# Kernel optimization log

Measured on AMD Instinct MI355X. Metric: run time of the kernel, lower is better.

## Reference

```python
import jax, jax.numpy as jnp
import numpy as np

N_EMBD = 1024
HEAD_SIZE = 64
WINDOW = 64
N_GLOBAL = 64
N_RANDOM = 64
B, T = 8, 2048


def setup_inputs() -> dict:
    key = jax.random.key(0)
    kx, kc, kk, kq, kv = jax.random.split(key, 5)
    x = jax.random.normal(kx, (B, T, N_EMBD), dtype=jnp.float32)
    random_cols = jax.random.randint(kc, (T, N_RANDOM), 0, T)
    s = 1.0 / np.sqrt(N_EMBD)
    Wk = jax.random.normal(kk, (HEAD_SIZE, N_EMBD), dtype=jnp.float32) * s
    Wq = jax.random.normal(kq, (HEAD_SIZE, N_EMBD), dtype=jnp.float32) * s
    Wv = jax.random.normal(kv, (HEAD_SIZE, N_EMBD), dtype=jnp.float32) * s
    return {"x": x, "random_cols": random_cols, "Wk": Wk, "Wq": Wq, "Wv": Wv}


def _bigbird_mask(Tlen, random_cols):
    rows = jnp.arange(Tlen)[:, None]
    cols = jnp.arange(Tlen)[None, :]
    causal = rows >= cols
    local = (cols >= rows - WINDOW + 1) & (cols <= rows)
    glob = (rows < N_GLOBAL) | (cols < N_GLOBAL)
    rand = jnp.zeros((Tlen, Tlen), dtype=bool).at[
        jnp.arange(Tlen)[:, None], random_cols].set(True)
    return (local | glob | rand) & causal  # [T, T] bool


def reference(x, random_cols, Wk, Wq, Wv):
    # projections (Linear, no bias): [B,T,C] @ [C,H] -> [B,T,H]
    k = jnp.einsum('btc,hc->bth', x, Wk)
    q = jnp.einsum('btc,hc->bth', x, Wq)
    v = jnp.einsum('btc,hc->bth', x, Wv)
    scale = 1.0 / jnp.sqrt(jnp.asarray(HEAD_SIZE, x.dtype))
    scores = jnp.einsum('bqh,bkh->bqk', q, k) * scale  # [B,T,T]
    mask = _bigbird_mask(x.shape[1], random_cols)
    scores = jnp.where(mask[None, :, :], scores, -jnp.inf)
    weights = jax.nn.softmax(scores, axis=-1)
    out = jnp.einsum('bqk,bkh->bqh', weights, v)  # [B,T,H]
    return out
```

## Files before the change

kernel.cpp:

```cpp
#include <hip/hip_runtime.h>
#include <math.h>

#define T_DIM 2048
#define C_DIM 1024
#define H_DIM 64
#define M_TOTAL 16384
#define NQKV 192

typedef __bf16 bf16x8 __attribute__((ext_vector_type(8)));
typedef float f32x4 __attribute__((ext_vector_type(4)));
typedef unsigned short u16x8 __attribute__((ext_vector_type(8)));

__device__ __forceinline__ unsigned short f2bf(float f) {
    unsigned u = __float_as_uint(f);
    unsigned r = (u + 0x7FFFu + ((u >> 16) & 1u)) >> 16;
    return (unsigned short)r;
}
__device__ __forceinline__ float bf2f(unsigned short u) {
    return __uint_as_float(((unsigned)u) << 16);
}
__device__ __forceinline__ unsigned pack_bf2(float f0, float f1) {
    unsigned u0 = __float_as_uint(f0) + 0x8000u;
    unsigned u1 = __float_as_uint(f1) + 0x8000u;
    return __builtin_amdgcn_perm(u1, u0, 0x07060302u);
}
__device__ __forceinline__ uint4 cvt8(float4 a, float4 b) {
    return make_uint4(pack_bf2(a.x, a.y), pack_bf2(a.z, a.w),
                      pack_bf2(b.x, b.y), pack_bf2(b.z, b.w));
}

__global__ __launch_bounds__(512) void proj_kernel(
    const float* __restrict__ x,
    const float* __restrict__ Wk,
    const float* __restrict__ Wq,
    const float* __restrict__ Wv,
    unsigned short* __restrict__ qkv)
{
    __shared__ unsigned short Ab[64 * 64];
    __shared__ unsigned short Bb[192 * 64];

    const int m0 = blockIdx.x * 64;
    const int t  = threadIdx.x;
    const int wv = t >> 6, ln = t & 63;
    const int mfr = ln & 15, kq = ln >> 4;
    const int r0 = (wv & 1) * 32;
    const int c0 = (wv >> 1) * 48;

    const int srow  = t >> 3;
    const int sk8   = (t & 7) * 8;
    const int skoff = sk8 ^ ((srow & 7) * 8);

    const float* gp[4] = {
        x  + (size_t)(m0 + srow) * C_DIM + sk8,
        Wk + (size_t)srow * C_DIM + sk8,
        Wq + (size_t)srow * C_DIM + sk8,
        Wv + (size_t)srow * C_DIM + sk8 };
    unsigned short* lp[4] = {
        &Ab[srow * 64 + skoff],
        &Bb[srow * 64 + skoff],
        &Bb[(srow + 64) * 64 + skoff],
        &Bb[(srow + 128) * 64 + skoff] };

    f32x4 acc[2][3] = {};

    float4 ra[4], rb[4];
    #pragma unroll
    for (int s = 0; s < 4; ++s) {
        ra[s] = *(const float4*)(gp[s]);
        rb[s] = *(const float4*)(gp[s] + 4);
    }

    for (int kc = 0; kc < C_DIM; kc += 64) {
        __syncthreads();
        #pragma unroll
        for (int s = 0; s < 4; ++s)
            *(uint4*)lp[s] = cvt8(ra[s], rb[s]);
        if (kc + 64 < C_DIM) {
            #pragma unroll
            for (int s = 0; s < 4; ++s) {
                ra[s] = *(const float4*)(gp[s] + kc + 64);
                rb[s] = *(const float4*)(gp[s] + kc + 68);
            }
        }
        __syncthreads();
        #pragma unroll
        for (int ks = 0; ks < 64; ks += 32) {
            bf16x8 af[2], bf[3];
            #pragma unroll
            for (int a = 0; a < 2; ++a) {
                int row = r0 + a * 16 + mfr;
                af[a] = *(const bf16x8*)&Ab[row * 64 + ((ks + kq * 8) ^ ((row & 7) * 8))];
            }
            #pragma unroll
            for (int b2 = 0; b2 < 3; ++b2) {
                int row = c0 + b2 * 16 + mfr;
                bf[b2] = *(const bf16x8*)&Bb[row * 64 + ((ks + kq * 8) ^ ((row & 7) * 8))];
            }
            #pragma unroll
            for (int a = 0; a < 2; ++a)
                #pragma unroll
                for (int b2 = 0; b2 < 3; ++b2)
                    acc[a][b2] = __builtin_amdgcn_mfma_f32_16x16x32_bf16(
                        af[a], bf[b2], acc[a][b2], 0, 0, 0);
        }
    }

    #pragma unroll
    for (int a = 0; a < 2; ++a)
        #pragma unroll
        for (int b2 = 0; b2 < 3; ++b2)
            #pragma unroll
            for (int r = 0; r < 4; ++r) {
                int row = m0 + r0 + a * 16 + kq * 4 + r;
                int col = c0 + b2 * 16 + mfr;
                qkv[(size_t)row * NQKV + col] = f2bf(acc[a][b2][r]);
            }
}

__global__ __launch_bounds__(256) void attn_kernel(
    const unsigned short* __restrict__ qkv,
    const int*  __restrict__ rnd,
    float* __restrict__ out)
{
    const int wv = threadIdx.x >> 6;
    const int ln = threadIdx.x & 63;
    const int b  = blockIdx.x & 7;
    const int i  = ((blockIdx.x >> 3) << 2) + wv;
    const int bi = b * T_DIM + i;

    __shared__ int2     cl_all[4][192];
    __shared__ unsigned bm_all[4][64];
    int2*     cl = cl_all[wv];
    unsigned* bm = bm_all[wv];

    bm[ln] = 0u;

    int  j0 = i - ln;            bool v0 = (j0 >= 0); if (!v0) j0 = 0;
    int  j1 = ln;                bool v1 = (j1 < i - 63);
    int  j2 = rnd[i * 64 + ln];  bool v2 = (j2 < i - 63) && (j2 >= 64);
    if (v2) {
        unsigned old = atomicOr(&bm[j2 >> 5], 1u << (j2 & 31));
        v2 = ((old >> (j2 & 31)) & 1u) == 0u;
    }
    cl[ln]       = make_int2(j0, 0);
    cl[64 + ln]  = make_int2(j1, 0);
    cl[128 + ln] = make_int2(j2, 0);

    const int e8 = (ln & 7) * 8;
    const int gg = ln >> 3;
    u16x8 qraw = *(const u16x8*)(qkv + (size_t)bi * NQKV + 64 + e8);
    float qr[8];
    #pragma unroll
    for (int e = 0; e < 8; ++e) qr[e] = bf2f(qraw[e]);

    const unsigned short* kb = qkv + (size_t)b * T_DIM * NQKV;

    #pragma unroll
    for (int n = 0; n < 24; n += 4) {
        int jj[4];
        #pragma unroll
        for (int u = 0; u < 4; ++u) jj[u] = cl[(n + u) * 8 + gg].x;
        u16x8 kv[4];
        #pragma unroll
        for (int u = 0; u < 4; ++u)
            kv[u] = *(const u16x8*)(kb + (size_t)jj[u] * NQKV + e8);
        #pragma unroll
        for (int u = 0; u < 4; ++u) {
            float p = 0.f;
            #pragma unroll
            for (int e = 0; e < 8; ++e) p = fmaf(qr[e], bf2f(kv[u][e]), p);
            p += __shfl_xor(p, 1);
            p += __shfl_xor(p, 2);
            p += __shfl_xor(p, 4);
            if ((ln & 7) == 0) cl[(n + u) * 8 + gg].y = __float_as_int(p);
        }
    }

    float s0 = __int_as_float(cl[ln].y);
    float s1 = __int_as_float(cl[64 + ln].y);
    float s2 = __int_as_float(cl[128 + ln].y);
    s0 = v0 ? s0 * 0.125f : -1e30f;
    s1 = v1 ? s1 * 0.125f : -1e30f;
    s2 = v2 ? s2 * 0.125f : -1e30f;

    float mx = fmaxf(s0, fmaxf(s1, s2));
    #pragma unroll
    for (int m = 32; m; m >>= 1) mx = fmaxf(mx, __shfl_xor(mx, m));
    float e0 = v0 ? __expf(s0 - mx) : 0.f;
    float e1 = v1 ? __expf(s1 - mx) : 0.f;
    float e2 = v2 ? __expf(s2 - mx) : 0.f;
    float sum = e0 + e1 + e2;
    #pragma unroll
    for (int m = 32; m; m >>= 1) sum += __shfl_xor(sum, m);

    cl[ln].y       = __float_as_int(e0);
    cl[64 + ln].y  = __float_as_int(e1);
    cl[128 + ln].y = __float_as_int(e2);

    const unsigned short* vb = kb + 128;
    float acc[8] = {};
    #pragma unroll
    for (int bt = 0; bt < 3; ++bt) {
        int2 p[8];
        #pragma unroll
        for (int c = 0; c < 8; ++c) p[c] = cl[(bt * 8 + c) * 8 + gg];
        u16x8 vvv[8];
        #pragma unroll
        for (int c = 0; c < 8; ++c)
            vvv[c] = *(const u16x8*)(vb + (size_t)p[c].x * NQKV + e8);
        #pragma unroll
        for (int c = 0; c < 8; ++c) {
            float w = __int_as_float(p[c].y);
            #pragma unroll
            for (int e = 0; e < 8; ++e)
                acc[e] = fmaf(w, bf2f(vvv[c][e]), acc[e]);
        }
    }
    #pragma unroll
    for (int m = 8; m <= 32; m <<= 1)
        #pragma unroll
        for (int e = 0; e < 8; ++e)
            acc[e] += __shfl_xor(acc[e], m);

    if (ln < 8) {
        float inv = 1.f / sum;
        float* op = &out[(size_t)bi * H_DIM + e8];
        *(float4*)op       = make_float4(acc[0]*inv, acc[1]*inv, acc[2]*inv, acc[3]*inv);
        *(float4*)(op + 4) = make_float4(acc[4]*inv, acc[5]*inv, acc[6]*inv, acc[7]*inv);
    }
}

extern "C" void kernel_launch(void* const* d_in, const int* in_sizes, int n_in,
                              void* d_out, int out_size, void* d_ws, size_t ws_size,
                              hipStream_t stream) {
    const float* x   = (const float*)d_in[0];
    const int*   rnd = (const int*)  d_in[1];
    const float* Wk  = (const float*)d_in[2];
    const float* Wq  = (const float*)d_in[3];
    const float* Wv  = (const float*)d_in[4];
    float* out = (float*)d_out;
    unsigned short* qkv = (unsigned short*)d_ws;

    proj_kernel<<<M_TOTAL / 64, 512, 0, stream>>>(x, Wk, Wq, Wv, qkv);
    attn_kernel<<<M_TOTAL / 4, 256, 0, stream>>>(qkv, rnd, out);
}
```

Before: 150.5 us.

## Stage global and local-window K/V rows in LDS shared by 16 queries per block

Each attention block now handles 16 consecutive queries (4 per wave) and first copies the 64 global-token K/V rows plus the union of their local-window rows into shared memory with a padded row stride. Local and global score and value gathers then read from LDS, and only the random columns still gather from global memory. This cuts repeated global and L2 traffic for the overlapping windows. In exchange it adds an up-front staging pass, a block-wide barrier, about 40 KB of LDS per block that may limit occupancy, and a quarter as many blocks.

```diff
diff --git a/kernel.cpp b/kernel.cpp
--- a/kernel.cpp
+++ b/kernel.cpp
@@ -6,6 +6,7 @@
 #define H_DIM 64
 #define M_TOTAL 16384
 #define NQKV 192
+#define LROW 140
 
 typedef __bf16 bf16x8 __attribute__((ext_vector_type(8)));
 typedef float f32x4 __attribute__((ext_vector_type(4)));
@@ -19,6 +20,8 @@
 __device__ __forceinline__ float bf2f(unsigned short u) {
     return __uint_as_float(((unsigned)u) << 16);
 }
+__device__ __forceinline__ float blo(unsigned u) { return __uint_as_float(u << 16); }
+__device__ __forceinline__ float bhi(unsigned u) { return __uint_as_float(u & 0xFFFF0000u); }
 __device__ __forceinline__ unsigned pack_bf2(float f0, float f1) {
     unsigned u0 = __float_as_uint(f0) + 0x8000u;
     unsigned u1 = __float_as_uint(f1) + 0x8000u;
@@ -122,111 +125,187 @@
     const int*  __restrict__ rnd,
     float* __restrict__ out)
 {
-    const int wv = threadIdx.x >> 6;
-    const int ln = threadIdx.x & 63;
-    const int b  = blockIdx.x & 7;
-    const int i  = ((blockIdx.x >> 3) << 2) + wv;
-    const int bi = b * T_DIM + i;
-
+    __shared__ unsigned short Ks[143 * LROW];
     __shared__ int2     cl_all[4][192];
     __shared__ unsigned bm_all[4][64];
+
+    const int t  = threadIdx.x;
+    const int wv = t >> 6;
+    const int ln = t & 63;
+    const int b  = blockIdx.x & 7;
+    const int i0 = (blockIdx.x >> 3) << 4;
+    const int Lb = (i0 - 63 > 64) ? (i0 - 63) : 64;
+    int nL = i0 + 16 - Lb; if (nL < 0) nL = 0;
+    const int S_rows = 64 + nL;
+
+    const unsigned short* kb = qkv + (size_t)b * T_DIM * NQKV;
+
+    {
+        const int u  = t >> 3;
+        const int c8 = (t & 7) * 8;
+        for (int s = u; s < S_rows; s += 32) {
+            int j = (s < 64) ? s : (Lb + (s - 64));
+            const unsigned short* src = kb + (size_t)j * NQKV;
+            uint4 kk = *(const uint4*)(src + c8);
+            uint4 vv = *(const uint4*)(src + 128 + c8);
+            *(uint2*)&Ks[s * LROW + c8]          = make_uint2(kk.x, kk.y);
+            *(uint2*)&Ks[s * LROW + c8 + 4]      = make_uint2(kk.z, kk.w);
+            *(uint2*)&Ks[s * LROW + 64 + c8]     = make_uint2(vv.x, vv.y);
+            *(uint2*)&Ks[s * LROW + 64 + c8 + 4] = make_uint2(vv.z, vv.w);
+        }
+    }
+    __syncthreads();
+
     int2*     cl = cl_all[wv];
     unsigned* bm = bm_all[wv];
-
-    bm[ln] = 0u;
-
-    int  j0 = i - ln;            bool v0 = (j0 >= 0); if (!v0) j0 = 0;
-    int  j1 = ln;                bool v1 = (j1 < i - 63);
-    int  j2 = rnd[i * 64 + ln];  bool v2 = (j2 < i - 63) && (j2 >= 64);
-    if (v2) {
-        unsigned old = atomicOr(&bm[j2 >> 5], 1u << (j2 & 31));
-        v2 = ((old >> (j2 & 31)) & 1u) == 0u;
-    }
-    cl[ln]       = make_int2(j0, 0);
-    cl[64 + ln]  = make_int2(j1, 0);
-    cl[128 + ln] = make_int2(j2, 0);
-
     const int e8 = (ln & 7) * 8;
     const int gg = ln >> 3;
-    u16x8 qraw = *(const u16x8*)(qkv + (size_t)bi * NQKV + 64 + e8);
-    float qr[8];
-    #pragma unroll
-    for (int e = 0; e < 8; ++e) qr[e] = bf2f(qraw[e]);
-
-    const unsigned short* kb = qkv + (size_t)b * T_DIM * NQKV;
-
-    #pragma unroll
-    for (int n = 0; n < 24; n += 4) {
-        int jj[4];
-        #pragma unroll
-        for (int u = 0; u < 4; ++u) jj[u] = cl[(n + u) * 8 + gg].x;
-        u16x8 kv[4];
-        #pragma unroll
-        for (int u = 0; u < 4; ++u)
-            kv[u] = *(const u16x8*)(kb + (size_t)jj[u] * NQKV + e8);
-        #pragma unroll
-        for (int u = 0; u < 4; ++u) {
-            float p = 0.f;
-            #pragma unroll
-            for (int e = 0; e < 8; ++e) p = fmaf(qr[e], bf2f(kv[u][e]), p);
-            p += __shfl_xor(p, 1);
-            p += __shfl_xor(p, 2);
-            p += __shfl_xor(p, 4);
-            if ((ln & 7) == 0) cl[(n + u) * 8 + gg].y = __float_as_int(p);
-        }
-    }
-
-    float s0 = __int_as_float(cl[ln].y);
-    float s1 = __int_as_float(cl[64 + ln].y);
-    float s2 = __int_as_float(cl[128 + ln].y);
-    s0 = v0 ? s0 * 0.125f : -1e30f;
-    s1 = v1 ? s1 * 0.125f : -1e30f;
-    s2 = v2 ? s2 * 0.125f : -1e30f;
-
-    float mx = fmaxf(s0, fmaxf(s1, s2));
-    #pragma unroll
-    for (int m = 32; m; m >>= 1) mx = fmaxf(mx, __shfl_xor(mx, m));
-    float e0 = v0 ? __expf(s0 - mx) : 0.f;
-    float e1 = v1 ? __expf(s1 - mx) : 0.f;
-    float e2 = v2 ? __expf(s2 - mx) : 0.f;
-    float sum = e0 + e1 + e2;
-    #pragma unroll
-    for (int m = 32; m; m >>= 1) sum += __shfl_xor(sum, m);
-
-    cl[ln].y       = __float_as_int(e0);
-    cl[64 + ln].y  = __float_as_int(e1);
-    cl[128 + ln].y = __float_as_int(e2);
-
-    const unsigned short* vb = kb + 128;
-    float acc[8] = {};
-    #pragma unroll
-    for (int bt = 0; bt < 3; ++bt) {
-        int2 p[8];
-        #pragma unroll
-        for (int c = 0; c < 8; ++c) p[c] = cl[(bt * 8 + c) * 8 + gg];
-        u16x8 vvv[8];
-        #pragma unroll
-        for (int c = 0; c < 8; ++c)
-            vvv[c] = *(const u16x8*)(vb + (size_t)p[c].x * NQKV + e8);
-        #pragma unroll
-        for (int c = 0; c < 8; ++c) {
-            float w = __int_as_float(p[c].y);
+
+    for (int qq = 0; qq < 4; ++qq) {
+        const int i  = i0 + wv * 4 + qq;
+        const int bi = b * T_DIM + i;
+
+        bm[ln] = 0u;
+
+        int  j0 = i - ln;            bool v0 = (j0 >= 0); if (!v0) j0 = 0;
+        int  j1 = ln;                bool v1 = (j1 < i - 63);
+        int  j2 = rnd[i * 64 + ln];  bool v2 = (j2 < i - 63) && (j2 >= 64);
+        if (v2) {
+            unsigned old = atomicOr(&bm[j2 >> 5], 1u << (j2 & 31));
+            v2 = ((old >> (j2 & 31)) & 1u) == 0u;
+        }
+        cl[ln]       = make_int2(j0, 0);
+        cl[64 + ln]  = make_int2(j1, 0);
+        cl[128 + ln] = make_int2(j2, 0);
+
+        uint4 qv4 = *(const uint4*)(qkv + (size_t)bi * NQKV + 64 + e8);
+        float qr[8] = { blo(qv4.x), bhi(qv4.x), blo(qv4.y), bhi(qv4.y),
+                        blo(qv4.z), bhi(qv4.z), blo(qv4.w), bhi(qv4.w) };
+
+        #pragma unroll
+        for (int n = 0; n < 16; n += 4) {
+            int sl[4];
+            #pragma unroll
+            for (int u = 0; u < 4; ++u) {
+                int j = cl[(n + u) * 8 + gg].x;
+                sl[u] = (j < 64) ? j : (64 + j - Lb);
+            }
+            uint2 ka[4], kc[4];
+            #pragma unroll
+            for (int u = 0; u < 4; ++u) {
+                ka[u] = *(const uint2*)&Ks[sl[u] * LROW + e8];
+                kc[u] = *(const uint2*)&Ks[sl[u] * LROW + e8 + 4];
+            }
+            #pragma unroll
+            for (int u = 0; u < 4; ++u) {
+                float p = 0.f;
+                p = fmaf(qr[0], blo(ka[u].x), p); p = fmaf(qr[1], bhi(ka[u].x), p);
+                p = fmaf(qr[2], blo(ka[u].y), p); p = fmaf(qr[3], bhi(ka[u].y), p);
+                p = fmaf(qr[4], blo(kc[u].x), p); p = fmaf(qr[5], bhi(kc[u].x), p);
+                p = fmaf(qr[6], blo(kc[u].y), p); p = fmaf(qr[7], bhi(kc[u].y), p);
+                p += __shfl_xor(p, 1);
+                p += __shfl_xor(p, 2);
+                p += __shfl_xor(p, 4);
+                if ((ln & 7) == 0) cl[(n + u) * 8 + gg].y = __float_as_int(p);
+            }
+        }
+        #pragma unroll
+        for (int n = 16; n < 24; n += 4) {
+            int jj[4];
+            #pragma unroll
+            for (int u = 0; u < 4; ++u) jj[u] = cl[(n + u) * 8 + gg].x;
+            u16x8 kv[4];
+            #pragma unroll
+            for (int u = 0; u < 4; ++u)
+                kv[u] = *(const u16x8*)(kb + (size_t)jj[u] * NQKV + e8);
+            #pragma unroll
+            for (int u = 0; u < 4; ++u) {
+                float p = 0.f;
+                #pragma unroll
+                for (int e = 0; e < 8; ++e) p = fmaf(qr[e], bf2f(kv[u][e]), p);
+                p += __shfl_xor(p, 1);
+                p += __shfl_xor(p, 2);
+                p += __shfl_xor(p, 4);
+                if ((ln & 7) == 0) cl[(n + u) * 8 + gg].y = __float_as_int(p);
+            }
+        }
+
+        float s0 = __int_as_float(cl[ln].y);
+        float s1 = __int_as_float(cl[64 + ln].y);
+        float s2 = __int_as_float(cl[128 + ln].y);
+        s0 = v0 ? s0 * 0.125f : -1e30f;
+        s1 = v1 ? s1 * 0.125f : -1e30f;
+        s2 = v2 ? s2 * 0.125f : -1e30f;
+
+        float mx = fmaxf(s0, fmaxf(s1, s2));
+        #pragma unroll
+        for (int m = 32; m; m >>= 1) mx = fmaxf(mx, __shfl_xor(mx, m));
+        float e0 = v0 ? __expf(s0 - mx) : 0.f;
+        float e1 = v1 ? __expf(s1 - mx) : 0.f;
+        float e2 = v2 ? __expf(s2 - mx) : 0.f;
+        float sum = e0 + e1 + e2;
+        #pragma unroll
+        for (int m = 32; m; m >>= 1) sum += __shfl_xor(sum, m);
+
+        cl[ln].y       = __float_as_int(e0);
+        cl[64 + ln].y  = __float_as_int(e1);
+        cl[128 + ln].y = __float_as_int(e2);
+
+        float acc[8] = {};
+        #pragma unroll
+        for (int bt = 0; bt < 2; ++bt) {
+            int2 p[8];
+            #pragma unroll
+            for (int c = 0; c < 8; ++c) p[c] = cl[(bt * 8 + c) * 8 + gg];
+            uint2 va[8], vc[8];
+            #pragma unroll
+            for (int c = 0; c < 8; ++c) {
+                int j = p[c].x;
+                int s = (j < 64) ? j : (64 + j - Lb);
+                va[c] = *(const uint2*)&Ks[s * LROW + 64 + e8];
+                vc[c] = *(const uint2*)&Ks[s * LROW + 64 + e8 + 4];
+            }
+            #pragma unroll
+            for (int c = 0; c < 8; ++c) {
+                float w = __int_as_float(p[c].y);
+                acc[0] = fmaf(w, blo(va[c].x), acc[0]);
+                acc[1] = fmaf(w, bhi(va[c].x), acc[1]);
+                acc[2] = fmaf(w, blo(va[c].y), acc[2]);
+                acc[3] = fmaf(w, bhi(va[c].y), acc[3]);
+                acc[4] = fmaf(w, blo(vc[c].x), acc[4]);
+                acc[5] = fmaf(w, bhi(vc[c].x), acc[5]);
+                acc[6] = fmaf(w, blo(vc[c].y), acc[6]);
+                acc[7] = fmaf(w, bhi(vc[c].y), acc[7]);
+            }
+        }
+        {
+            int2 p[8];
+            #pragma unroll
+            for (int c = 0; c < 8; ++c) p[c] = cl[(16 + c) * 8 + gg];
+            u16x8 vvv[8];
+            #pragma unroll
+            for (int c = 0; c < 8; ++c)
+                vvv[c] = *(const u16x8*)(kb + (size_t)p[c].x * NQKV + 128 + e8);
+            #pragma unroll
+            for (int c = 0; c < 8; ++c) {
+                float w = __int_as_float(p[c].y);
+                #pragma unroll
+                for (int e = 0; e < 8; ++e)
+                    acc[e] = fmaf(w, bf2f(vvv[c][e]), acc[e]);
+            }
+        }
+        #pragma unroll
+        for (int m = 8; m <= 32; m <<= 1)
             #pragma unroll
             for (int e = 0; e < 8; ++e)
-                acc[e] = fmaf(w, bf2f(vvv[c][e]), acc[e]);
-        }
-    }
-    #pragma unroll
-    for (int m = 8; m <= 32; m <<= 1)
-        #pragma unroll
-        for (int e = 0; e < 8; ++e)
-            acc[e] += __shfl_xor(acc[e], m);
-
-    if (ln < 8) {
-        float inv = 1.f / sum;
-        float* op = &out[(size_t)bi * H_DIM + e8];
-        *(float4*)op       = make_float4(acc[0]*inv, acc[1]*inv, acc[2]*inv, acc[3]*inv);
-        *(float4*)(op + 4) = make_float4(acc[4]*inv, acc[5]*inv, acc[6]*inv, acc[7]*inv);
+                acc[e] += __shfl_xor(acc[e], m);
+
+        if (ln < 8) {
+            float inv = 1.f / sum;
+            float* op = &out[(size_t)bi * H_DIM + e8];
+            *(float4*)op       = make_float4(acc[0]*inv, acc[1]*inv, acc[2]*inv, acc[3]*inv);
+            *(float4*)(op + 4) = make_float4(acc[4]*inv, acc[5]*inv, acc[6]*inv, acc[7]*inv);
+        }
     }
 }
 
@@ -242,5 +321,5 @@
     unsigned short* qkv = (unsigned short*)d_ws;
 
     proj_kernel<<<M_TOTAL / 64, 512, 0, stream>>>(x, Wk, Wq, Wv, qkv);
-    attn_kernel<<<M_TOTAL / 4, 256, 0, stream>>>(qkv, rnd, out);
-}
+    attn_kernel<<<M_TOTAL / 16, 256, 0, stream>>>(qkv, rnd, out);
+}
```

New measurement: 179.6 us. +19.4%, slower.

## Process two adjacent query rows per wavefront sharing window and global K/V loads

Applied to the files above, without the earlier changes.

Each wavefront now handles two consecutive query rows, loading the 65-row union of their sliding windows and the 64 global rows of K and V once and applying them to both queries. Random columns are still gathered separately for each row. The grid is halved to match. The aim is to cut redundant gathered K/V memory traffic and the per-row setup overhead. In exchange it raises register and LDS use per wave and halves the number of blocks, which may reduce occupancy and latency hiding.

```diff
diff --git a/kernel.cpp b/kernel.cpp
--- a/kernel.cpp
+++ b/kernel.cpp
@@ -125,108 +125,292 @@
     const int wv = threadIdx.x >> 6;
     const int ln = threadIdx.x & 63;
     const int b  = blockIdx.x & 7;
-    const int i  = ((blockIdx.x >> 3) << 2) + wv;
-    const int bi = b * T_DIM + i;
-
-    __shared__ int2     cl_all[4][192];
-    __shared__ unsigned bm_all[4][64];
-    int2*     cl = cl_all[wv];
-    unsigned* bm = bm_all[wv];
-
-    bm[ln] = 0u;
-
-    int  j0 = i - ln;            bool v0 = (j0 >= 0); if (!v0) j0 = 0;
-    int  j1 = ln;                bool v1 = (j1 < i - 63);
-    int  j2 = rnd[i * 64 + ln];  bool v2 = (j2 < i - 63) && (j2 >= 64);
-    if (v2) {
-        unsigned old = atomicOr(&bm[j2 >> 5], 1u << (j2 & 31));
-        v2 = ((old >> (j2 & 31)) & 1u) == 0u;
-    }
-    cl[ln]       = make_int2(j0, 0);
-    cl[64 + ln]  = make_int2(j1, 0);
-    cl[128 + ln] = make_int2(j2, 0);
+    const int iA = ((blockIdx.x >> 3) << 3) + wv * 2;
+    const int iB = iA + 1;
+    const int biA = b * T_DIM + iA;
+
+    __shared__ int2     clA_all[4][192], clB_all[4][192];
+    __shared__ unsigned bmA_all[4][64],  bmB_all[4][64];
+    int2*     clA = clA_all[wv];
+    int2*     clB = clB_all[wv];
+    unsigned* bmA = bmA_all[wv];
+    unsigned* bmB = bmB_all[wv];
+
+    bmA[ln] = 0u;
+    bmB[ln] = 0u;
+
+    int  j0A = iA - ln;            bool v0A = (j0A >= 0);
+    int  j0B = iB - ln;            bool v0B = (j0B >= 0);
+    bool v1A = (ln < iA - 63);
+    bool v1B = (ln < iB - 63);
+    int  j2A = rnd[iA * 64 + ln];  bool v2A = (j2A < iA - 63) && (j2A >= 64);
+    int  j2B = rnd[iB * 64 + ln];  bool v2B = (j2B < iB - 63) && (j2B >= 64);
+    if (v2A) {
+        unsigned old = atomicOr(&bmA[j2A >> 5], 1u << (j2A & 31));
+        v2A = ((old >> (j2A & 31)) & 1u) == 0u;
+    }
+    if (v2B) {
+        unsigned old = atomicOr(&bmB[j2B >> 5], 1u << (j2B & 31));
+        v2B = ((old >> (j2B & 31)) & 1u) == 0u;
+    }
+    clA[128 + ln] = make_int2(j2A, 0);
+    clB[128 + ln] = make_int2(j2B, 0);
 
     const int e8 = (ln & 7) * 8;
     const int gg = ln >> 3;
-    u16x8 qraw = *(const u16x8*)(qkv + (size_t)bi * NQKV + 64 + e8);
-    float qr[8];
-    #pragma unroll
-    for (int e = 0; e < 8; ++e) qr[e] = bf2f(qraw[e]);
+    u16x8 qrawA = *(const u16x8*)(qkv + (size_t)biA * NQKV + 64 + e8);
+    u16x8 qrawB = *(const u16x8*)(qkv + (size_t)(biA + 1) * NQKV + 64 + e8);
+    float qA[8], qB[8];
+    #pragma unroll
+    for (int e = 0; e < 8; ++e) { qA[e] = bf2f(qrawA[e]); qB[e] = bf2f(qrawB[e]); }
 
     const unsigned short* kb = qkv + (size_t)b * T_DIM * NQKV;
 
     #pragma unroll
-    for (int n = 0; n < 24; n += 4) {
-        int jj[4];
-        #pragma unroll
-        for (int u = 0; u < 4; ++u) jj[u] = cl[(n + u) * 8 + gg].x;
+    for (int n0 = 0; n0 < 9; n0 += 3) {
+        const int nn = (n0 + 3 <= 9) ? 3 : (9 - n0);
+        int rr[3]; u16x8 kv[3];
+        #pragma unroll
+        for (int u = 0; u < 3; ++u) {
+            if (u < nn) {
+                rr[u] = (n0 + u) * 8 + gg;
+                int j = iA - 63 + rr[u];
+                int jc = j < 0 ? 0 : (j > T_DIM - 1 ? T_DIM - 1 : j);
+                kv[u] = *(const u16x8*)(kb + (size_t)jc * NQKV + e8);
+            }
+        }
+        #pragma unroll
+        for (int u = 0; u < 3; ++u) {
+            if (u < nn) {
+                float pA = 0.f, pB = 0.f;
+                #pragma unroll
+                for (int e = 0; e < 8; ++e) {
+                    float kvf = bf2f(kv[u][e]);
+                    pA = fmaf(qA[e], kvf, pA);
+                    pB = fmaf(qB[e], kvf, pB);
+                }
+                pA += __shfl_xor(pA, 1); pB += __shfl_xor(pB, 1);
+                pA += __shfl_xor(pA, 2); pB += __shfl_xor(pB, 2);
+                pA += __shfl_xor(pA, 4); pB += __shfl_xor(pB, 4);
+                if ((ln & 7) == 0) {
+                    int lA = 63 - rr[u];
+                    int lB = 64 - rr[u];
+                    if (lA >= 0)            clA[lA].y = __float_as_int(pA);
+                    if (lB >= 0 && lB < 64) clB[lB].y = __float_as_int(pB);
+                }
+            }
+        }
+    }
+
+    #pragma unroll
+    for (int n0 = 0; n0 < 8; n0 += 4) {
         u16x8 kv[4];
         #pragma unroll
         for (int u = 0; u < 4; ++u)
+            kv[u] = *(const u16x8*)(kb + (size_t)((n0 + u) * 8 + gg) * NQKV + e8);
+        #pragma unroll
+        for (int u = 0; u < 4; ++u) {
+            float pA = 0.f, pB = 0.f;
+            #pragma unroll
+            for (int e = 0; e < 8; ++e) {
+                float kvf = bf2f(kv[u][e]);
+                pA = fmaf(qA[e], kvf, pA);
+                pB = fmaf(qB[e], kvf, pB);
+            }
+            pA += __shfl_xor(pA, 1); pB += __shfl_xor(pB, 1);
+            pA += __shfl_xor(pA, 2); pB += __shfl_xor(pB, 2);
+            pA += __shfl_xor(pA, 4); pB += __shfl_xor(pB, 4);
+            if ((ln & 7) == 0) {
+                int j = (n0 + u) * 8 + gg;
+                clA[64 + j].y = __float_as_int(pA);
+                clB[64 + j].y = __float_as_int(pB);
+            }
+        }
+    }
+
+    #pragma unroll
+    for (int n0 = 16; n0 < 24; n0 += 4) {
+        int jj[4]; u16x8 kv[4];
+        #pragma unroll
+        for (int u = 0; u < 4; ++u) jj[u] = clA[(n0 + u) * 8 + gg].x;
+        #pragma unroll
+        for (int u = 0; u < 4; ++u)
             kv[u] = *(const u16x8*)(kb + (size_t)jj[u] * NQKV + e8);
         #pragma unroll
         for (int u = 0; u < 4; ++u) {
             float p = 0.f;
             #pragma unroll
-            for (int e = 0; e < 8; ++e) p = fmaf(qr[e], bf2f(kv[u][e]), p);
-            p += __shfl_xor(p, 1);
-            p += __shfl_xor(p, 2);
-            p += __shfl_xor(p, 4);
-            if ((ln & 7) == 0) cl[(n + u) * 8 + gg].y = __float_as_int(p);
-        }
-    }
-
-    float s0 = __int_as_float(cl[ln].y);
-    float s1 = __int_as_float(cl[64 + ln].y);
-    float s2 = __int_as_float(cl[128 + ln].y);
-    s0 = v0 ? s0 * 0.125f : -1e30f;
-    s1 = v1 ? s1 * 0.125f : -1e30f;
-    s2 = v2 ? s2 * 0.125f : -1e30f;
-
-    float mx = fmaxf(s0, fmaxf(s1, s2));
-    #pragma unroll
-    for (int m = 32; m; m >>= 1) mx = fmaxf(mx, __shfl_xor(mx, m));
-    float e0 = v0 ? __expf(s0 - mx) : 0.f;
-    float e1 = v1 ? __expf(s1 - mx) : 0.f;
-    float e2 = v2 ? __expf(s2 - mx) : 0.f;
-    float sum = e0 + e1 + e2;
-    #pragma unroll
-    for (int m = 32; m; m >>= 1) sum += __shfl_xor(sum, m);
-
-    cl[ln].y       = __float_as_int(e0);
-    cl[64 + ln].y  = __float_as_int(e1);
-    cl[128 + ln].y = __float_as_int(e2);
+            for (int e = 0; e < 8; ++e) p = fmaf(qA[e], bf2f(kv[u][e]), p);
+            p += __shfl_xor(p, 1); p += __shfl_xor(p, 2); p += __shfl_xor(p, 4);
+            if ((ln & 7) == 0) clA[(n0 + u) * 8 + gg].y = __float_as_int(p);
+        }
+    }
+    #pragma unroll
+    for (int n0 = 16; n0 < 24; n0 += 4) {
+        int jj[4]; u16x8 kv[4];
+        #pragma unroll
+        for (int u = 0; u < 4; ++u) jj[u] = clB[(n0 + u) * 8 + gg].x;
+        #pragma unroll
+        for (int u = 0; u < 4; ++u)
+            kv[u] = *(const u16x8*)(kb + (size_t)jj[u] * NQKV + e8);
+        #pragma unroll
+        for (int u = 0; u < 4; ++u) {
+            float p = 0.f;
+            #pragma unroll
+            for (int e = 0; e < 8; ++e) p = fmaf(qB[e], bf2f(kv[u][e]), p);
+            p += __shfl_xor(p, 1); p += __shfl_xor(p, 2); p += __shfl_xor(p, 4);
+            if ((ln & 7) == 0) clB[(n0 + u) * 8 + gg].y = __float_as_int(p);
+        }
+    }
+
+    float sumA, sumB;
+    {
+        float s0 = __int_as_float(clA[ln].y);
+        float s1 = __int_as_float(clA[64 + ln].y);
+        float s2 = __int_as_float(clA[128 + ln].y);
+        s0 = v0A ? s0 * 0.125f : -1e30f;
+        s1 = v1A ? s1 * 0.125f : -1e30f;
+        s2 = v2A ? s2 * 0.125f : -1e30f;
+        float mx = fmaxf(s0, fmaxf(s1, s2));
+        #pragma unroll
+        for (int m = 32; m; m >>= 1) mx = fmaxf(mx, __shfl_xor(mx, m));
+        float e0 = v0A ? __expf(s0 - mx) : 0.f;
+        float e1 = v1A ? __expf(s1 - mx) : 0.f;
+        float e2 = v2A ? __expf(s2 - mx) : 0.f;
+        float sm = e0 + e1 + e2;
+        #pragma unroll
+        for (int m = 32; m; m >>= 1) sm += __shfl_xor(sm, m);
+        sumA = sm;
+        clA[ln].y       = __float_as_int(e0);
+        clA[64 + ln].y  = __float_as_int(e1);
+        clA[128 + ln].y = __float_as_int(e2);
+    }
+    {
+        float s0 = __int_as_float(clB[ln].y);
+        float s1 = __int_as_float(clB[64 + ln].y);
+        float s2 = __int_as_float(clB[128 + ln].y);
+        s0 = v0B ? s0 * 0.125f : -1e30f;
+        s1 = v1B ? s1 * 0.125f : -1e30f;
+        s2 = v2B ? s2 * 0.125f : -1e30f;
+        float mx = fmaxf(s0, fmaxf(s1, s2));
+        #pragma unroll
+        for (int m = 32; m; m >>= 1) mx = fmaxf(mx, __shfl_xor(mx, m));
+        float e0 = v0B ? __expf(s0 - mx) : 0.f;
+        float e1 = v1B ? __expf(s1 - mx) : 0.f;
+        float e2 = v2B ? __expf(s2 - mx) : 0.f;
+        float sm = e0 + e1 + e2;
+        #pragma unroll
+        for (int m = 32; m; m >>= 1) sm += __shfl_xor(sm, m);
+        sumB = sm;
+        clB[ln].y       = __float_as_int(e0);
+        clB[64 + ln].y  = __float_as_int(e1);
+        clB[128 + ln].y = __float_as_int(e2);
+    }
 
     const unsigned short* vb = kb + 128;
-    float acc[8] = {};
-    #pragma unroll
-    for (int bt = 0; bt < 3; ++bt) {
-        int2 p[8];
-        #pragma unroll
-        for (int c = 0; c < 8; ++c) p[c] = cl[(bt * 8 + c) * 8 + gg];
-        u16x8 vvv[8];
-        #pragma unroll
-        for (int c = 0; c < 8; ++c)
-            vvv[c] = *(const u16x8*)(vb + (size_t)p[c].x * NQKV + e8);
-        #pragma unroll
-        for (int c = 0; c < 8; ++c) {
-            float w = __int_as_float(p[c].y);
+    float accA[8] = {}, accB[8] = {};
+
+    #pragma unroll
+    for (int n0 = 0; n0 < 9; n0 += 3) {
+        const int nn = (n0 + 3 <= 9) ? 3 : (9 - n0);
+        int rr[3]; u16x8 vv[3];
+        #pragma unroll
+        for (int u = 0; u < 3; ++u) {
+            if (u < nn) {
+                rr[u] = (n0 + u) * 8 + gg;
+                int j = iA - 63 + rr[u];
+                int jc = j < 0 ? 0 : (j > T_DIM - 1 ? T_DIM - 1 : j);
+                vv[u] = *(const u16x8*)(vb + (size_t)jc * NQKV + e8);
+            }
+        }
+        #pragma unroll
+        for (int u = 0; u < 3; ++u) {
+            if (u < nn) {
+                int lA = 63 - rr[u];
+                int lB = 64 - rr[u];
+                int lAc = lA < 0 ? 0 : lA;
+                int lBc = (lB < 0) ? 0 : (lB > 63 ? 63 : lB);
+                float wA = __int_as_float(clA[lAc].y);
+                float wB = __int_as_float(clB[lBc].y);
+                wA = (lA >= 0) ? wA : 0.f;
+                wB = (lB >= 0 && lB < 64) ? wB : 0.f;
+                #pragma unroll
+                for (int e = 0; e < 8; ++e) {
+                    float vf = bf2f(vv[u][e]);
+                    accA[e] = fmaf(wA, vf, accA[e]);
+                    accB[e] = fmaf(wB, vf, accB[e]);
+                }
+            }
+        }
+    }
+    #pragma unroll
+    for (int n0 = 0; n0 < 8; n0 += 4) {
+        u16x8 vv[4];
+        #pragma unroll
+        for (int u = 0; u < 4; ++u)
+            vv[u] = *(const u16x8*)(vb + (size_t)((n0 + u) * 8 + gg) * NQKV + e8);
+        #pragma unroll
+        for (int u = 0; u < 4; ++u) {
+            int j = (n0 + u) * 8 + gg;
+            float wA = __int_as_float(clA[64 + j].y);
+            float wB = __int_as_float(clB[64 + j].y);
+            #pragma unroll
+            for (int e = 0; e < 8; ++e) {
+                float vf = bf2f(vv[u][e]);
+                accA[e] = fmaf(wA, vf, accA[e]);
+                accB[e] = fmaf(wB, vf, accB[e]);
+            }
+        }
+    }
+    #pragma unroll
+    for (int n0 = 16; n0 < 24; n0 += 4) {
+        int2 p[4]; u16x8 vv[4];
+        #pragma unroll
+        for (int u = 0; u < 4; ++u) p[u] = clA[(n0 + u) * 8 + gg];
+        #pragma unroll
+        for (int u = 0; u < 4; ++u)
+            vv[u] = *(const u16x8*)(vb + (size_t)p[u].x * NQKV + e8);
+        #pragma unroll
+        for (int u = 0; u < 4; ++u) {
+            float w = __int_as_float(p[u].y);
             #pragma unroll
             for (int e = 0; e < 8; ++e)
-                acc[e] = fmaf(w, bf2f(vvv[c][e]), acc[e]);
-        }
-    }
+                accA[e] = fmaf(w, bf2f(vv[u][e]), accA[e]);
+        }
+    }
+    #pragma unroll
+    for (int n0 = 16; n0 < 24; n0 += 4) {
+        int2 p[4]; u16x8 vv[4];
+        #pragma unroll
+        for (int u = 0; u < 4; ++u) p[u] = clB[(n0 + u) * 8 + gg];
+        #pragma unroll
+        for (int u = 0; u < 4; ++u)
+            vv[u] = *(const u16x8*)(vb + (size_t)p[u].x * NQKV + e8);
+        #pragma unroll
+        for (int u = 0; u < 4; ++u) {
+            float w = __int_as_float(p[u].y);
+            #pragma unroll
+            for (int e = 0; e < 8; ++e)
+                accB[e] = fmaf(w, bf2f(vv[u][e]), accB[e]);
+        }
+    }
+
     #pragma unroll
     for (int m = 8; m <= 32; m <<= 1)
         #pragma unroll
-        for (int e = 0; e < 8; ++e)
-            acc[e] += __shfl_xor(acc[e], m);
+        for (int e = 0; e < 8; ++e) {
+            accA[e] += __shfl_xor(accA[e], m);
+            accB[e] += __shfl_xor(accB[e], m);
+        }
 
     if (ln < 8) {
-        float inv = 1.f / sum;
-        float* op = &out[(size_t)bi * H_DIM + e8];
-        *(float4*)op       = make_float4(acc[0]*inv, acc[1]*inv, acc[2]*inv, acc[3]*inv);
-        *(float4*)(op + 4) = make_float4(acc[4]*inv, acc[5]*inv, acc[6]*inv, acc[7]*inv);
+        float invA = 1.f / sumA, invB = 1.f / sumB;
+        float* opA = &out[(size_t)biA * H_DIM + e8];
+        *(float4*)opA       = make_float4(accA[0]*invA, accA[1]*invA, accA[2]*invA, accA[3]*invA);
+        *(float4*)(opA + 4) = make_float4(accA[4]*invA, accA[5]*invA, accA[6]*invA, accA[7]*invA);
+        float* opB = &out[(size_t)(biA + 1) * H_DIM + e8];
+        *(float4*)opB       = make_float4(accB[0]*invB, accB[1]*invB, accB[2]*invB, accB[3]*invB);
+        *(float4*)(opB + 4) = make_float4(accB[4]*invB, accB[5]*invB, accB[6]*invB, accB[7]*invB);
     }
 }
 
@@ -242,5 +426,5 @@
     unsigned short* qkv = (unsigned short*)d_ws;
 
     proj_kernel<<<M_TOTAL / 64, 512, 0, stream>>>(x, Wk, Wq, Wv, qkv);
-    attn_kernel<<<M_TOTAL / 4, 256, 0, stream>>>(qkv, rnd, out);
-}
+    attn_kernel<<<M_TOTAL / 8, 256, 0, stream>>>(qkv, rnd, out);
+}
```

Result: slower. 167.0 us (+11.0%).
